# Kernel optimization log

Measured on AMD Instinct MI355X. Metric: run time of the kernel, lower is better.

## Reference

```python
import jax, jax.numpy as jnp
import numpy as np

SEQ_LEN = 4096
D_IN = 1024
D_OUT = 1024


def setup_inputs() -> dict:
    key = jax.random.key(0)
    k_x, k_q, k_k, k_v = jax.random.split(key, 4)
    s = 1.0 / np.sqrt(D_IN)
    return {
        "x": jax.random.normal(k_x, (SEQ_LEN, D_IN), dtype=jnp.float32),
        "W_query": jax.random.normal(k_q, (D_IN, D_OUT), dtype=jnp.float32) * s,
        "W_key": jax.random.normal(k_k, (D_IN, D_OUT), dtype=jnp.float32) * s,
        "W_value": jax.random.normal(k_v, (D_IN, D_OUT), dtype=jnp.float32) * s,
    }


def reference(x, W_query, W_key, W_value):
    # QKV projections (Linear without bias): [S, d_out]
    q = x @ W_query
    k = x @ W_key
    v = x @ W_value
    # Full S x S score matrix, causal mask, scaled softmax
    scores = q @ k.T  # [S, S]
    seq_len = x.shape[0]
    causal = jnp.tril(jnp.ones((seq_len, seq_len), dtype=bool))
    scores = jnp.where(causal, scores, -jnp.inf)
    scale = 1.0 / jnp.sqrt(jnp.asarray(k.shape[-1], dtype=scores.dtype))
    attn = jax.nn.softmax(scores * scale, axis=-1)
    return attn @ v  # [S, d_out]
```

## Files before the change

kernel.cpp:

```cpp
#include <hip/hip_runtime.h>
#include <math.h>

#define SEQ 4096
#define DIM 1024

typedef unsigned short u16;
typedef __attribute__((ext_vector_type(8))) short short8;
typedef __attribute__((ext_vector_type(4))) float floatx4;
typedef __attribute__((ext_vector_type(4))) unsigned short us4;

__device__ __forceinline__ float bf2f(u16 u) {
    union { unsigned int i; float f; } c; c.i = ((unsigned int)u) << 16; return c.f;
}
__device__ __forceinline__ u16 f2bf(float f) {
    union { float f; unsigned int i; } c; c.f = f;
    return (u16)((c.i + 0x7fffu + ((c.i >> 16) & 1u)) >> 16);
}
__device__ __forceinline__ void gload_lds16(const u16* g, u16* l) {
    __builtin_amdgcn_global_load_lds((const __attribute__((address_space(1))) void*)g,
                                     (__attribute__((address_space(3))) void*)l, 16, 0, 0);
}

template <int MODE>
__global__ __launch_bounds__(256) void gemm_nt(const u16* __restrict__ A,
                                               const u16* __restrict__ B,
                                               void* __restrict__ Cv,
                                               float* __restrict__ Ppart,
                                               u16* __restrict__ VtOut,
                                               float* __restrict__ Lsum,
                                               int lda, int ldb, int ldc, int Kdim,
                                               float scale0) {
    const int row0 = blockIdx.y * 128;
    const int col0 = blockIdx.x * 128;
    if (MODE == 1 && col0 > row0) return;
    int kbeg = 0, kend = Kdim, chunk = 0;
    if (MODE == 2) {
        chunk = blockIdx.z;
        kbeg = chunk << 10;
        const int klim = row0 + 128;
        if (kbeg >= klim) return;
        kend = min(kbeg + 1024, klim);
    }

    __shared__ u16 As[3][4096];
    __shared__ u16 Bs[3][4096];

    const int tid  = threadIdx.x;
    const int wave = tid >> 6;
    const int lane = tid & 63;
    const int wm = wave & 1;
    const int wn = wave >> 1;

    const int s0 = wave * 128 + lane;
    const int s1 = s0 + 64;
    const int r0s = s0 >> 2, q0s = ((s0 & 3) ^ ((s0 >> 3) & 3)) * 8;
    const int r1s = s1 >> 2, q1s = ((s1 & 3) ^ ((s1 >> 3) & 3)) * 8;
    const u16* aP0 = A + (size_t)(row0 + r0s) * lda + kbeg + q0s;
    const u16* aP1 = A + (size_t)(row0 + r1s) * lda + kbeg + q1s;
    const u16* bP0 = B + (size_t)(col0 + r0s) * ldb + kbeg + q0s;
    const u16* bP1 = B + (size_t)(col0 + r1s) * ldb + kbeg + q1s;
    const int l0 = wave * 1024;

    floatx4 acc[4][4] = {};
    const int niter = (kend - kbeg) >> 5;
    const int frow = lane & 15;
    const int xq = (((lane >> 4) ^ ((frow >> 1) & 3))) * 8;

    gload_lds16(aP0, &As[0][l0]);
    gload_lds16(aP1, &As[0][l0 + 512]);
    gload_lds16(bP0, &Bs[0][l0]);
    gload_lds16(bP1, &Bs[0][l0 + 512]);
    aP0 += 32; aP1 += 32; bP0 += 32; bP1 += 32;
    gload_lds16(aP0, &As[1][l0]);
    gload_lds16(aP1, &As[1][l0 + 512]);
    gload_lds16(bP0, &Bs[1][l0]);
    gload_lds16(bP1, &Bs[1][l0 + 512]);
    aP0 += 32; aP1 += 32; bP0 += 32; bP1 += 32;

    auto compute_tile = [&](int c) {
        short8 af[4], bfr[4];
#pragma unroll
        for (int t = 0; t < 4; ++t) {
            af[t]  = *(const short8*)&As[c][(wm * 64 + t * 16 + frow) * 32 + xq];
            bfr[t] = *(const short8*)&Bs[c][(wn * 64 + t * 16 + frow) * 32 + xq];
        }
#pragma unroll
        for (int mt = 0; mt < 4; ++mt)
#pragma unroll
            for (int nt = 0; nt < 4; ++nt)
                acc[mt][nt] = __builtin_amdgcn_mfma_f32_16x16x32_bf16(
                    af[mt], bfr[nt], acc[mt][nt], 0, 0, 0);
    };

    int cur = 0, pre = 2;
    for (int it = 0; it < niter - 2; ++it) {
        asm volatile("s_waitcnt vmcnt(4)\n\ts_barrier" ::: "memory");
        short8 af[4], bfr[4];
#pragma unroll
        for (int t = 0; t < 4; ++t) {
            af[t]  = *(const short8*)&As[cur][(wm * 64 + t * 16 + frow) * 32 + xq];
            bfr[t] = *(const short8*)&Bs[cur][(wn * 64 + t * 16 + frow) * 32 + xq];
        }
        gload_lds16(aP0, &As[pre][l0]);
        gload_lds16(aP1, &As[pre][l0 + 512]);
        gload_lds16(bP0, &Bs[pre][l0]);
        gload_lds16(bP1, &Bs[pre][l0 + 512]);
        aP0 += 32; aP1 += 32; bP0 += 32; bP1 += 32;
#pragma unroll
        for (int mt = 0; mt < 4; ++mt)
#pragma unroll
            for (int nt = 0; nt < 4; ++nt)
                acc[mt][nt] = __builtin_amdgcn_mfma_f32_16x16x32_bf16(
                    af[mt], bfr[nt], acc[mt][nt], 0, 0, 0);
        cur = (cur == 2) ? 0 : cur + 1;
        pre = (pre == 2) ? 0 : pre + 1;
    }
    asm volatile("s_waitcnt vmcnt(4)\n\ts_barrier" ::: "memory");
    compute_tile(cur);
    cur = (cur == 2) ? 0 : cur + 1;
    asm volatile("s_waitcnt vmcnt(0)\n\ts_barrier" ::: "memory");
    compute_tile(cur);

    const int cr = (lane >> 4) * 4;
    const int cc = lane & 15;
    if (MODE == 1) {
        u16* dst = (u16*)Cv;
#pragma unroll
        for (int mt = 0; mt < 4; ++mt) {
#pragma unroll
            for (int r = 0; r < 4; ++r) {
                const int grow = row0 + wm * 64 + mt * 16 + cr + r;
                float rowsum = 0.f;
#pragma unroll
                for (int nt = 0; nt < 4; ++nt) {
                    const int gcol = col0 + wn * 64 + nt * 16 + cc;
                    const float e = (gcol <= grow) ? __expf(acc[mt][nt][r]) : 0.f;
                    rowsum += e;
                    dst[(size_t)grow * ldc + gcol] = f2bf(e);
                }
                rowsum += __shfl_xor(rowsum, 1);
                rowsum += __shfl_xor(rowsum, 2);
                rowsum += __shfl_xor(rowsum, 4);
                rowsum += __shfl_xor(rowsum, 8);
                if (cc == 0) atomicAdd(&Lsum[grow], rowsum);
            }
        }
    } else if (MODE == 2) {
        float* dst;
        if (chunk == 0) {
            dst = (float*)Cv;
        } else {
            const ptrdiff_t poff[3] = {0, (ptrdiff_t)3072 * 1024, (ptrdiff_t)5120 * 1024};
            dst = Ppart + poff[chunk - 1] - (ptrdiff_t)(chunk << 10) * 1024;
        }
#pragma unroll
        for (int mt = 0; mt < 4; ++mt)
#pragma unroll
            for (int r = 0; r < 4; ++r) {
                const int grow = row0 + wm * 64 + mt * 16 + cr + r;
                const float invl = 1.0f / Lsum[grow];
#pragma unroll
                for (int nt = 0; nt < 4; ++nt) {
                    const int col = col0 + wn * 64 + nt * 16 + cc;
                    dst[(size_t)grow * ldc + col] = acc[mt][nt][r] * invl;
                }
            }
    } else if (MODE == 0 && col0 >= 2048) {
#pragma unroll
        for (int mt = 0; mt < 4; ++mt)
#pragma unroll
            for (int nt = 0; nt < 4; ++nt) {
                const int row = row0 + wm * 64 + mt * 16 + cr;
                const int col = (col0 - 2048) + wn * 64 + nt * 16 + cc;
                us4 o = { f2bf(acc[mt][nt][0]), f2bf(acc[mt][nt][1]),
                          f2bf(acc[mt][nt][2]), f2bf(acc[mt][nt][3]) };
                *(us4*)&VtOut[(size_t)col * SEQ + row] = o;
            }
    } else {
        u16* dst = (u16*)Cv;
        const float sc = (col0 < 1024) ? scale0 : 1.0f;
#pragma unroll
        for (int mt = 0; mt < 4; ++mt)
#pragma unroll
            for (int nt = 0; nt < 4; ++nt)
#pragma unroll
                for (int r = 0; r < 4; ++r) {
                    const int row = row0 + wm * 64 + mt * 16 + cr + r;
                    const int col = col0 + wn * 64 + nt * 16 + cc;
                    dst[(size_t)row * ldc + col] = f2bf(acc[mt][nt][r] * sc);
                }
    }
}

__global__ __launch_bounds__(256) void transpose_cast(const float* __restrict__ W0,
                                                      const float* __restrict__ W1,
                                                      const float* __restrict__ W2,
                                                      u16* __restrict__ Wt) {
    __shared__ float tile[32][33];
    const float* W = (blockIdx.z == 0) ? W0 : (blockIdx.z == 1) ? W1 : W2;
    u16* out = Wt + (size_t)blockIdx.z * DIM * DIM;
    const int bx = blockIdx.x * 32;
    const int by = blockIdx.y * 32;
    const int tx = threadIdx.x & 31;
    const int ty = (threadIdx.x >> 5) * 4;
#pragma unroll
    for (int r = 0; r < 4; ++r)
        tile[ty + r][tx] = W[(size_t)(by + ty + r) * DIM + bx + tx];
    __syncthreads();
#pragma unroll
    for (int r = 0; r < 4; ++r)
        out[(size_t)(bx + ty + r) * DIM + by + tx] = f2bf(tile[tx][ty + r]);
}

__global__ __launch_bounds__(256) void cast_bf16(const float* __restrict__ X,
                                                 u16* __restrict__ Xb,
                                                 float* __restrict__ Lsum) {
    if (blockIdx.x < 16) Lsum[blockIdx.x * 256 + threadIdx.x] = 0.f;
    const size_t i = ((size_t)blockIdx.x * 256 + threadIdx.x) * 4;
    const float4 v = *(const float4*)(X + i);
    us4 o = { f2bf(v.x), f2bf(v.y), f2bf(v.z), f2bf(v.w) };
    *(us4*)(Xb + i) = o;
}

__global__ __launch_bounds__(256) void reduce_pv(float* __restrict__ O,
                                                 const float* __restrict__ P) {
    const int r = blockIdx.x;
    const int row = 1024 + r;
    const int col = threadIdx.x * 4;
    float4 a = *(const float4*)(O + (size_t)row * 1024 + col);
    const float4 b1 = *(const float4*)(P + (size_t)r * 1024 + col);
    a.x += b1.x; a.y += b1.y; a.z += b1.z; a.w += b1.w;
    if (row >= 2048) {
        const float4 b2 = *(const float4*)(P + (size_t)3072 * 1024 +
                                           (size_t)(row - 2048) * 1024 + col);
        a.x += b2.x; a.y += b2.y; a.z += b2.z; a.w += b2.w;
    }
    if (row >= 3072) {
        const float4 b3 = *(const float4*)(P + (size_t)5120 * 1024 +
                                           (size_t)(row - 3072) * 1024 + col);
        a.x += b3.x; a.y += b3.y; a.z += b3.z; a.w += b3.w;
    }
    *(float4*)(O + (size_t)row * 1024 + col) = a;
}

extern "C" void kernel_launch(void* const* d_in, const int* in_sizes, int n_in,
                              void* d_out, int out_size, void* d_ws, size_t ws_size,
                              hipStream_t stream) {
    const float* x  = (const float*)d_in[0];
    const float* Wq = (const float*)d_in[1];
    const float* Wk = (const float*)d_in[2];
    const float* Wv = (const float*)d_in[3];

    u16* xb    = (u16*)d_ws;
    u16* Wt    = xb  + (size_t)SEQ * DIM;
    u16* QK    = Wt  + (size_t)3072 * DIM;
    u16* Vt    = QK  + (size_t)SEQ * 2048;
    u16* E     = Vt  + (size_t)DIM * SEQ;
    float* Ppart = (float*)(E + (size_t)SEQ * SEQ);
    float* Lsum  = Ppart + (size_t)8192 * 1024;

    cast_bf16<<<SEQ * DIM / 1024, 256, 0, stream>>>(x, xb, Lsum);
    transpose_cast<<<dim3(32, 32, 3), 256, 0, stream>>>(Wq, Wk, Wv, Wt);

    gemm_nt<0><<<dim3(24, 32), 256, 0, stream>>>(
        xb, Wt, QK, nullptr, Vt, nullptr, DIM, DIM, 2048, DIM, 0.03125f);

    gemm_nt<1><<<dim3(32, 32), 256, 0, stream>>>(
        QK, QK + 1024, E, nullptr, nullptr, Lsum, 2048, 2048, SEQ, DIM, 1.0f);

    gemm_nt<2><<<dim3(8, 32, 4), 256, 0, stream>>>(
        E, Vt, d_out, Ppart, nullptr, Lsum, SEQ, SEQ, DIM, SEQ, 1.0f);

    reduce_pv<<<3072, 256, 0, stream>>>((float*)d_out, Ppart);
}
```

Measured before the change: 201.9 us.

## Fuse prep kernels, compact causal grids, replace split-K reduction with atomics

Merges the x cast, the weight transpose-casts and the output/Lsum zeroing into one prep launch. The score GEMM now launches only the 528 lower-triangular tiles, mapped from a linear index. The PV GEMM launches only the valid (row, k-chunk) tiles and accumulates into the output with float atomicAdd. This drops the partial buffer and the reduce kernel, saving launches and empty blocks, at the cost of atomic traffic and a nondeterministic summation order.

```diff
diff --git a/kernel.cpp b/kernel.cpp
--- a/kernel.cpp
+++ b/kernel.cpp
@@ -25,21 +25,33 @@
 __global__ __launch_bounds__(256) void gemm_nt(const u16* __restrict__ A,
                                                const u16* __restrict__ B,
                                                void* __restrict__ Cv,
-                                               float* __restrict__ Ppart,
                                                u16* __restrict__ VtOut,
                                                float* __restrict__ Lsum,
                                                int lda, int ldb, int ldc, int Kdim,
                                                float scale0) {
-    const int row0 = blockIdx.y * 128;
-    const int col0 = blockIdx.x * 128;
-    if (MODE == 1 && col0 > row0) return;
-    int kbeg = 0, kend = Kdim, chunk = 0;
-    if (MODE == 2) {
-        chunk = blockIdx.z;
-        kbeg = chunk << 10;
-        const int klim = row0 + 128;
-        if (kbeg >= klim) return;
-        kend = min(kbeg + 1024, klim);
+    int row0, col0, kbeg = 0, kend = Kdim;
+    if (MODE == 1) {
+        const int t = blockIdx.x;
+        int by = (int)((sqrtf(8.0f * t + 1.0f) - 1.0f) * 0.5f);
+        while ((by + 1) * (by + 2) / 2 <= t) ++by;
+        while (by * (by + 1) / 2 > t) --by;
+        const int bx = t - by * (by + 1) / 2;
+        row0 = by * 128;
+        col0 = bx * 128;
+    } else if (MODE == 2) {
+        col0 = blockIdx.x * 128;
+        const int u = blockIdx.y;
+        int r, c;
+        if (u < 32)      { c = 0; r = u; }
+        else if (u < 56) { c = 1; r = u - 24; }
+        else if (u < 72) { c = 2; r = u - 40; }
+        else             { c = 3; r = u - 48; }
+        row0 = r * 128;
+        kbeg = c << 10;
+        kend = min(kbeg + 1024, row0 + 128);
+    } else {
+        row0 = blockIdx.y * 128;
+        col0 = blockIdx.x * 128;
     }
 
     __shared__ u16 As[3][4096];
@@ -146,13 +158,7 @@
             }
         }
     } else if (MODE == 2) {
-        float* dst;
-        if (chunk == 0) {
-            dst = (float*)Cv;
-        } else {
-            const ptrdiff_t poff[3] = {0, (ptrdiff_t)3072 * 1024, (ptrdiff_t)5120 * 1024};
-            dst = Ppart + poff[chunk - 1] - (ptrdiff_t)(chunk << 10) * 1024;
-        }
+        float* O = (float*)Cv;
 #pragma unroll
         for (int mt = 0; mt < 4; ++mt)
 #pragma unroll
@@ -162,7 +168,7 @@
 #pragma unroll
                 for (int nt = 0; nt < 4; ++nt) {
                     const int col = col0 + wn * 64 + nt * 16 + cc;
-                    dst[(size_t)grow * ldc + col] = acc[mt][nt][r] * invl;
+                    atomicAdd(&O[(size_t)grow * ldc + col], acc[mt][nt][r] * invl);
                 }
             }
     } else if (MODE == 0 && col0 >= 2048) {
@@ -192,55 +198,46 @@
     }
 }
 
-__global__ __launch_bounds__(256) void transpose_cast(const float* __restrict__ W0,
-                                                      const float* __restrict__ W1,
-                                                      const float* __restrict__ W2,
-                                                      u16* __restrict__ Wt) {
+__global__ __launch_bounds__(256) void prep(const float* __restrict__ x,
+                                            const float* __restrict__ W0,
+                                            const float* __restrict__ W1,
+                                            const float* __restrict__ W2,
+                                            u16* __restrict__ xb,
+                                            u16* __restrict__ Wt,
+                                            float* __restrict__ O,
+                                            float* __restrict__ Lsum) {
     __shared__ float tile[32][33];
-    const float* W = (blockIdx.z == 0) ? W0 : (blockIdx.z == 1) ? W1 : W2;
-    u16* out = Wt + (size_t)blockIdx.z * DIM * DIM;
-    const int bx = blockIdx.x * 32;
-    const int by = blockIdx.y * 32;
-    const int tx = threadIdx.x & 31;
-    const int ty = (threadIdx.x >> 5) * 4;
-#pragma unroll
-    for (int r = 0; r < 4; ++r)
-        tile[ty + r][tx] = W[(size_t)(by + ty + r) * DIM + bx + tx];
-    __syncthreads();
-#pragma unroll
-    for (int r = 0; r < 4; ++r)
-        out[(size_t)(bx + ty + r) * DIM + by + tx] = f2bf(tile[tx][ty + r]);
-}
-
-__global__ __launch_bounds__(256) void cast_bf16(const float* __restrict__ X,
-                                                 u16* __restrict__ Xb,
-                                                 float* __restrict__ Lsum) {
-    if (blockIdx.x < 16) Lsum[blockIdx.x * 256 + threadIdx.x] = 0.f;
-    const size_t i = ((size_t)blockIdx.x * 256 + threadIdx.x) * 4;
-    const float4 v = *(const float4*)(X + i);
-    us4 o = { f2bf(v.x), f2bf(v.y), f2bf(v.z), f2bf(v.w) };
-    *(us4*)(Xb + i) = o;
-}
-
-__global__ __launch_bounds__(256) void reduce_pv(float* __restrict__ O,
-                                                 const float* __restrict__ P) {
-    const int r = blockIdx.x;
-    const int row = 1024 + r;
-    const int col = threadIdx.x * 4;
-    float4 a = *(const float4*)(O + (size_t)row * 1024 + col);
-    const float4 b1 = *(const float4*)(P + (size_t)r * 1024 + col);
-    a.x += b1.x; a.y += b1.y; a.z += b1.z; a.w += b1.w;
-    if (row >= 2048) {
-        const float4 b2 = *(const float4*)(P + (size_t)3072 * 1024 +
-                                           (size_t)(row - 2048) * 1024 + col);
-        a.x += b2.x; a.y += b2.y; a.z += b2.z; a.w += b2.w;
-    }
-    if (row >= 3072) {
-        const float4 b3 = *(const float4*)(P + (size_t)5120 * 1024 +
-                                           (size_t)(row - 3072) * 1024 + col);
-        a.x += b3.x; a.y += b3.y; a.z += b3.z; a.w += b3.w;
-    }
-    *(float4*)(O + (size_t)row * 1024 + col) = a;
+    const int b = blockIdx.x;
+    const int tid = threadIdx.x;
+    if (b < 4096) {
+        const size_t i = ((size_t)b * 256 + tid) * 4;
+        const float4 v = *(const float4*)(x + i);
+        us4 o = { f2bf(v.x), f2bf(v.y), f2bf(v.z), f2bf(v.w) };
+        *(us4*)(xb + i) = o;
+    } else if (b < 7168) {
+        const int t = b - 4096;
+        const int z = t >> 10;
+        const int idx = t & 1023;
+        const float* W = (z == 0) ? W0 : (z == 1) ? W1 : W2;
+        u16* out = Wt + (size_t)z * DIM * DIM;
+        const int bx = (idx & 31) * 32;
+        const int by = (idx >> 5) * 32;
+        const int tx = tid & 31;
+        const int ty = (tid >> 5) * 4;
+#pragma unroll
+        for (int r = 0; r < 4; ++r)
+            tile[ty + r][tx] = W[(size_t)(by + ty + r) * DIM + bx + tx];
+        __syncthreads();
+#pragma unroll
+        for (int r = 0; r < 4; ++r)
+            out[(size_t)(bx + ty + r) * DIM + by + tx] = f2bf(tile[tx][ty + r]);
+    } else {
+        const int t = b - 7168;
+        const size_t i = ((size_t)t * 256 + tid) * 4;
+        *(float4*)(O + i) = make_float4(0.f, 0.f, 0.f, 0.f);
+        if (t < 4) *(float4*)(Lsum + (size_t)(t * 256 + tid) * 4) =
+            make_float4(0.f, 0.f, 0.f, 0.f);
+    }
 }
 
 extern "C" void kernel_launch(void* const* d_in, const int* in_sizes, int n_in,
@@ -256,20 +253,16 @@
     u16* QK    = Wt  + (size_t)3072 * DIM;
     u16* Vt    = QK  + (size_t)SEQ * 2048;
     u16* E     = Vt  + (size_t)DIM * SEQ;
-    float* Ppart = (float*)(E + (size_t)SEQ * SEQ);
-    float* Lsum  = Ppart + (size_t)8192 * 1024;
-
-    cast_bf16<<<SEQ * DIM / 1024, 256, 0, stream>>>(x, xb, Lsum);
-    transpose_cast<<<dim3(32, 32, 3), 256, 0, stream>>>(Wq, Wk, Wv, Wt);
+    float* Lsum = (float*)(E + (size_t)SEQ * SEQ);
+
+    prep<<<8192, 256, 0, stream>>>(x, Wq, Wk, Wv, xb, Wt, (float*)d_out, Lsum);
 
     gemm_nt<0><<<dim3(24, 32), 256, 0, stream>>>(
-        xb, Wt, QK, nullptr, Vt, nullptr, DIM, DIM, 2048, DIM, 0.03125f);
-
-    gemm_nt<1><<<dim3(32, 32), 256, 0, stream>>>(
-        QK, QK + 1024, E, nullptr, nullptr, Lsum, 2048, 2048, SEQ, DIM, 1.0f);
-
-    gemm_nt<2><<<dim3(8, 32, 4), 256, 0, stream>>>(
-        E, Vt, d_out, Ppart, nullptr, Lsum, SEQ, SEQ, DIM, SEQ, 1.0f);
-
-    reduce_pv<<<3072, 256, 0, stream>>>((float*)d_out, Ppart);
-}
+        xb, Wt, QK, Vt, nullptr, DIM, DIM, 2048, DIM, 0.03125f);
+
+    gemm_nt<1><<<528, 256, 0, stream>>>(
+        QK, QK + 1024, E, nullptr, Lsum, 2048, 2048, SEQ, DIM, 1.0f);
+
+    gemm_nt<2><<<dim3(8, 80), 256, 0, stream>>>(
+        E, Vt, d_out, nullptr, Lsum, SEQ, SEQ, DIM, SEQ, 1.0f);
+}
```

New measurement: 197.7 us. 1.02x faster.
